# Performance work log

Measured on AMD Instinct MI355X. Metric: run time of the kernel, lower is better.

The kernel has to match this reference:

```python
import jax, jax.numpy as jnp
import numpy as np

N, E, IN, HID, G, OUT = 50000, 800000, 9, 128, 256, 10
CLUSTERS, NCO, MCO = 20, 6, 4  # numerator deg 5 (6 coeffs), denominator deg 4
EPS = 1e-5


def _gcn(x, W, b, src, dst):
    # PyG GCNConv: x' = D^-1/2 (A + I) D^-1/2 (x W) + b, with self-loops
    n = x.shape[0]
    h = x @ W  # [N, out]
    ones = jnp.ones(src.shape[0], h.dtype)
    deg = jax.ops.segment_sum(ones, dst, num_segments=n) + 1.0  # + self-loop
    dinv = jax.lax.rsqrt(deg)
    coef = (dinv[src] * dinv[dst])[:, None]
    agg = jax.ops.segment_sum(h[src] * coef, dst, num_segments=n)
    agg = agg + h * (dinv * dinv)[:, None]  # self-loop messages
    return agg + b


def _rational(x, num, den, assign):
    # per-cluster safe Pade rational: P_5(x) / (1 + |Q_4(x)|), coeffs gathered per channel
    a = num[assign]  # [HID, 6]
    q = den[assign]  # [HID, 4]
    P = a[:, 5]
    for i in (4, 3, 2, 1, 0):
        P = P * x + a[:, i]
    Q = q[:, 3]
    for i in (2, 1, 0):
        Q = Q * x + q[:, i]
    Q = Q * x  # Q has no constant term
    return P / (1.0 + jnp.abs(Q))


def _bn(x, g, b):
    m = x.mean(axis=0)
    v = x.var(axis=0)
    return g * (x - m) * jax.lax.rsqrt(v + EPS) + b


def setup_inputs() -> dict:
    key = jax.random.key(0)
    ks = jax.random.split(key, 32)
    d = {}
    d["x"] = jax.random.normal(ks[0], (N, IN), jnp.float32)
    d["edge_index"] = jax.random.randint(ks[1], (2, E), 0, N, jnp.int32)
    d["batch"] = jnp.sort(jax.random.randint(ks[2], (N,), 0, G, jnp.int32))
    dims = [(IN, HID), (HID, HID), (HID, HID), (HID, HID)]
    for i, (di, do) in enumerate(dims):
        d[f"W{i}"] = jax.random.normal(ks[3 + i], (di, do), jnp.float32) / np.sqrt(di)
        d[f"b{i}"] = jnp.zeros((do,), jnp.float32)
        d[f"g{i}"] = jnp.ones((do,), jnp.float32)
        d[f"be{i}"] = jnp.zeros((do,), jnp.float32)
    d["rat_num"] = jax.random.normal(ks[10], (CLUSTERS, NCO), jnp.float32) * 0.3
    d["rat_den"] = jax.random.normal(ks[11], (CLUSTERS, MCO), jnp.float32) * 0.3
    d["cluster_assign"] = (jnp.arange(HID) % CLUSTERS).astype(jnp.int32)
    d["HW1"] = jax.random.normal(ks[12], (HID, HID), jnp.float32) / np.sqrt(HID)
    d["Hb1"] = jnp.zeros((HID,), jnp.float32)
    d["HW2"] = jax.random.normal(ks[13], (HID, HID), jnp.float32) / np.sqrt(HID)
    d["Hb2"] = jnp.zeros((HID,), jnp.float32)
    d["HW3"] = jax.random.normal(ks[14], (HID, OUT), jnp.float32) / np.sqrt(HID)
    d["Hb3"] = jnp.zeros((OUT,), jnp.float32)
    return d


def reference(x, edge_index, batch,
              W0, b0, g0, be0, W1, b1, g1, be1,
              W2, b2, g2, be2, W3, b3, g3, be3,
              rat_num, rat_den, cluster_assign,
              HW1, Hb1, HW2, Hb2, HW3, Hb3):
    src, dst = edge_index[0], edge_index[1]
    h = x
    for W, b, g, be in ((W0, b0, g0, be0), (W1, b1, g1, be1),
                        (W2, b2, g2, be2), (W3, b3, g3, be3)):
        h = _gcn(h, W, b, src, dst)
        h = _rational(h, rat_num, rat_den, cluster_assign)
        h = _bn(h, g, be)
        # Dropout(p=0.1): identity in eval mode
    # global mean pool over graphs
    counts = jax.ops.segment_sum(jnp.ones((h.shape[0],), h.dtype), batch, num_segments=G)
    pooled = jax.ops.segment_sum(h, batch, num_segments=G) / jnp.maximum(counts, 1.0)[:, None]
    # MLP head: (Dropout->Linear->GELU) x2, Dropout->Linear
    z = jax.nn.gelu(pooled @ HW1 + Hb1, approximate=False)
    z = jax.nn.gelu(z @ HW2 + Hb2, approximate=False)
    return z @ HW3 + Hb3
```

## Files before the change

kernel.cpp:

```cpp
#include <hip/hip_runtime.h>
#include <math.h>

#define HID 128
#define GRP 256
#define INF 9
#define OUTF 10
#define NPART 8

typedef _Float16 half8 __attribute__((ext_vector_type(8)));
typedef _Float16 h2 __attribute__((ext_vector_type(2)));
typedef __attribute__((ext_vector_type(4))) float f32x4;

__device__ __forceinline__ int2 nt_load_int2(const int2* p) {
    long long v = __builtin_nontemporal_load((const long long*)p);
    int2 r; r.x = (int)(v & 0xffffffffLL); r.y = (int)(v >> 32);
    return r;
}

__global__ void hist_prepw_kernel(const int* __restrict__ ei, int* __restrict__ cnt_part,
                                  int E, int n,
                                  const float* __restrict__ W1, const float* __restrict__ W2,
                                  const float* __restrict__ W3,
                                  _Float16* __restrict__ Whi, _Float16* __restrict__ Wlo) {
    int e = blockIdx.x * 256 + threadIdx.x;
    if (e < E) atomicAdd(&cnt_part[(size_t)(blockIdx.x & 7) * n + ei[E + e]], 1);
    if (blockIdx.x < 192) {
        int l = blockIdx.x >> 6;
        int idx = (blockIdx.x & 63) * 256 + threadIdx.x;
        const float* W = (l == 0) ? W1 : (l == 1) ? W2 : W3;
        int nn = idx >> 7, k = idx & 127;
        float w = W[k * HID + nn];
        _Float16 hi = (_Float16)w;
        _Float16 lo = (_Float16)(w - (float)hi);
        int nt = nn >> 4, l16 = nn & 15;
        int kc = k >> 5, quad = (k >> 3) & 3, j = k & 7;
        size_t off = (size_t)(l + 1) * HID * HID +
                     ((((nt * 4 + kc) * 4 + quad) * 16 + l16) * 8 + j);
        Whi[off] = hi;
        Wlo[off] = lo;
    }
}

__global__ __launch_bounds__(256) void scanA_kernel(const int* __restrict__ cnt_part,
                                                    int* __restrict__ bsum, int n) {
    int tid = threadIdx.x;
    int base = blockIdx.x * 1024 + tid * 4;
    int s = 0;
    #pragma unroll
    for (int i = 0; i < 4; i++) {
        int idx = base + i;
        if (idx < n) {
            #pragma unroll
            for (int x = 0; x < NPART; x++) s += cnt_part[(size_t)x * n + idx];
        }
    }
    #pragma unroll
    for (int off = 32; off > 0; off >>= 1) s += __shfl_down(s, off);
    __shared__ int ws[4];
    if ((tid & 63) == 0) ws[tid >> 6] = s;
    __syncthreads();
    if (tid == 0) bsum[blockIdx.x] = ws[0] + ws[1] + ws[2] + ws[3];
}

__global__ void scanB_kernel(int* __restrict__ bsum, int* __restrict__ row_ptr,
                             int nb, int n) {
    int lane = threadIdx.x;
    int carry = 0;
    for (int base = 0; base < nb; base += 64) {
        int v = (base + lane < nb) ? bsum[base + lane] : 0;
        int ps = v;
        #pragma unroll
        for (int off = 1; off < 64; off <<= 1) {
            int t = __shfl_up(ps, off);
            if (lane >= off) ps += t;
        }
        if (base + lane < nb) bsum[base + lane] = carry + ps - v;
        carry += __shfl(ps, 63);
    }
    if (lane == 0) row_ptr[n] = carry;
}

__global__ __launch_bounds__(256) void scanC_kernel(const int* __restrict__ cnt_part,
                                                    const int* __restrict__ bsum,
                                                    const int* __restrict__ batch,
                                                    int* __restrict__ row_ptr,
                                                    int* __restrict__ cursor_part,
                                                    float* __restrict__ dinv,
                                                    int* __restrict__ gstart,
                                                    int* __restrict__ gend, int n) {
    int tid = threadIdx.x;
    int lane = tid & 63, wid = tid >> 6;
    int idx0 = blockIdx.x * 1024 + tid * 4;
    int v[4];
    #pragma unroll
    for (int i = 0; i < 4; i++) {
        int idx = idx0 + i;
        int s = 0;
        if (idx < n) {
            #pragma unroll
            for (int x = 0; x < NPART; x++) s += cnt_part[(size_t)x * n + idx];
        }
        v[i] = s;
    }
    int s = v[0] + v[1] + v[2] + v[3];
    int ps = s;
    #pragma unroll
    for (int off = 1; off < 64; off <<= 1) {
        int t = __shfl_up(ps, off);
        if (lane >= off) ps += t;
    }
    __shared__ int wsum[4];
    if (lane == 63) wsum[wid] = ps;
    __syncthreads();
    int woff = 0;
    #pragma unroll
    for (int i = 0; i < 4; i++) if (i < wid) woff += wsum[i];
    int run = bsum[blockIdx.x] + woff + (ps - s);
    #pragma unroll
    for (int i = 0; i < 4; i++) {
        int idx = idx0 + i;
        if (idx < n) {
            row_ptr[idx] = run;
            dinv[idx] = rsqrtf((float)(v[i] + 1));
            int b = run;
            #pragma unroll
            for (int x = 0; x < NPART; x++) {
                cursor_part[(size_t)x * n + idx] = b;
                b += cnt_part[(size_t)x * n + idx];
            }
            run += v[i];
            int bt = batch[idx];
            if (idx == 0 || batch[idx - 1] != bt) gstart[bt] = idx;
            if (idx == n - 1 || batch[idx + 1] != bt) gend[bt] = idx + 1;
        }
    }
}

__global__ void fill_kernel(const int* __restrict__ ei, int* __restrict__ cursor_part,
                            const float* __restrict__ dinv,
                            int2* __restrict__ csr, int E, int n) {
    int e = blockIdx.x * blockDim.x + threadIdx.x;
    if (e >= E) return;
    int s = ei[e], d = ei[E + e];
    int pos = atomicAdd(&cursor_part[(size_t)(blockIdx.x & 7) * n + d], 1);
    long long v = ((long long)__float_as_int(dinv[s] * dinv[d]) << 32) | (unsigned)s;
    *(long long*)&csr[pos] = v;
}

__global__ __launch_bounds__(256) void statreduce_kernel(const float* __restrict__ part,
                                                         int nb, float* __restrict__ statOut) {
    int j = blockIdx.x;
    int tid = threadIdx.x;
    float s = 0.0f;
    for (int b = tid; b < nb; b += 256) s += part[(size_t)b * 256 + j];
    #pragma unroll
    for (int off = 32; off > 0; off >>= 1) s += __shfl_down(s, off);
    __shared__ float ws[4];
    if ((tid & 63) == 0) ws[tid >> 6] = s;
    __syncthreads();
    if (tid == 0) statOut[j] = ws[0] + ws[1] + ws[2] + ws[3];
}

__device__ __forceinline__ float rational_act(float xv, const float* __restrict__ a,
                                              const float* __restrict__ q) {
    float P = a[5];
    P = fmaf(P, xv, a[4]); P = fmaf(P, xv, a[3]); P = fmaf(P, xv, a[2]);
    P = fmaf(P, xv, a[1]); P = fmaf(P, xv, a[0]);
    float Q = q[3];
    Q = fmaf(Q, xv, q[2]); Q = fmaf(Q, xv, q[1]); Q = fmaf(Q, xv, q[0]);
    Q *= xv;
    return P / (1.0f + fabsf(Q));
}

__global__ __launch_bounds__(256) void aggx_kernel(const float* __restrict__ x,
                                                   const int* __restrict__ row_ptr,
                                                   const int2* __restrict__ csr,
                                                   const float* __restrict__ dinv,
                                                   float* __restrict__ aggX,
                                                   float* __restrict__ cagg, int n) {
    int tid = threadIdx.x;
    int node = blockIdx.x * 16 + (tid >> 4);
    int lane = tid & 15;
    if (node >= n) return;
    float di = dinv[node];
    float self = di * di;
    float acc = (lane < INF) ? x[node * INF + lane] * self : 0.0f;
    float cfs = self;
    int beg = row_ptr[node], end = row_ptr[node + 1];
    for (int j = beg; j < end; j++) {
        int2 p = nt_load_int2(&csr[j]);
        float cf = __int_as_float(p.y);
        cfs += cf;
        if (lane < INF) acc = fmaf(cf, x[p.x * INF + lane], acc);
    }
    if (lane < INF) aggX[node * INF + lane] = acc;
    if (lane == 0) cagg[node] = cfs;
}

__global__ __launch_bounds__(256) void gemm0_fused_kernel(const float* __restrict__ aggX,
                                                          const float* __restrict__ W0,
                                                          const float* __restrict__ b0,
                                                          const float* __restrict__ rat_num,
                                                          const float* __restrict__ rat_den,
                                                          const int* __restrict__ cl_assign,
                                                          _Float16* __restrict__ act,
                                                          float* __restrict__ part, int n) {
    __shared__ float Ws[INF * HID];
    __shared__ float s_num[120], s_den[80];
    __shared__ int s_cl[HID];
    __shared__ float s_b[HID];
    __shared__ float s_sum[HID], s_sq[HID];
    int tid = threadIdx.x;
    for (int i = tid; i < INF * HID; i += 256) Ws[i] = W0[i];
    if (tid < 120) s_num[tid] = rat_num[tid];
    if (tid < 80) s_den[tid] = rat_den[tid];
    if (tid < HID) {
        s_cl[tid] = cl_assign[tid];
        s_b[tid] = b0[tid];
        s_sum[tid] = 0.0f; s_sq[tid] = 0.0f;
    }
    __syncthreads();
    int w = tid >> 6, lane = tid & 63;
    int c0 = lane * 2, c1 = c0 + 1;
    const float* a0 = s_num + s_cl[c0] * 6;
    const float* q0 = s_den + s_cl[c0] * 4;
    const float* a1 = s_num + s_cl[c1] * 6;
    const float* q1 = s_den + s_cl[c1] * 4;
    float psum0 = 0.0f, psq0 = 0.0f, psum1 = 0.0f, psq1 = 0.0f;
    for (int node = blockIdx.x * 4 + w; node < n; node += gridDim.x * 4) {
        float xv[INF];
        #pragma unroll
        for (int k = 0; k < INF; k++) xv[k] = aggX[node * INF + k];
        float acc0 = s_b[c0], acc1 = s_b[c1];
        #pragma unroll
        for (int k = 0; k < INF; k++) {
            acc0 = fmaf(xv[k], Ws[k * HID + c0], acc0);
            acc1 = fmaf(xv[k], Ws[k * HID + c1], acc1);
        }
        float r0 = rational_act(acc0, a0, q0);
        float r1 = rational_act(acc1, a1, q1);
        h2 o; o[0] = (_Float16)r0; o[1] = (_Float16)r1;
        __builtin_nontemporal_store(o, (h2*)&act[(size_t)node * HID + c0]);
        psum0 += r0; psq0 = fmaf(r0, r0, psq0);
        psum1 += r1; psq1 = fmaf(r1, r1, psq1);
    }
    atomicAdd(&s_sum[c0], psum0);
    atomicAdd(&s_sq[c0], psq0);
    atomicAdd(&s_sum[c1], psum1);
    atomicAdd(&s_sq[c1], psq1);
    __syncthreads();
    float pv = (tid < 128) ? s_sum[tid] : s_sq[tid - 128];
    __builtin_nontemporal_store(pv, &part[(size_t)blockIdx.x * 256 + tid]);
}

__global__ __launch_bounds__(256, 5) void layer_fused_kernel(const _Float16* __restrict__ act,
                                                          const int2* __restrict__ csr,
                                                          const int* __restrict__ row_ptr,
                                                          const float* __restrict__ dinv,
                                                          const float* __restrict__ cagg,
                                                          const float* __restrict__ statPrev,
                                                          const float* __restrict__ gPrev,
                                                          const float* __restrict__ bePrev,
                                                          const _Float16* __restrict__ Whi,
                                                          const _Float16* __restrict__ Wlo,
                                                          const float* __restrict__ bias,
                                                          const float* __restrict__ rat_num,
                                                          const float* __restrict__ rat_den,
                                                          const int* __restrict__ cl_assign,
                                                          _Float16* __restrict__ actOut,
                                                          float* __restrict__ part, int n) {
    __shared__ _Float16 Alds[16 * 136];
    __shared__ float s_bnw[HID], s_bnu[HID];
    __shared__ float s_num[120], s_den[80];
    __shared__ int s_cl[HID];
    __shared__ float s_bias[HID];
    __shared__ float s_sum[HID], s_sq[HID];
    int tid = threadIdx.x;
    if (tid < 120) s_num[tid] = rat_num[tid];
    if (tid < 80) s_den[tid] = rat_den[tid];
    if (tid < HID) {
        float inv_n = 1.0f / (float)n;
        float mean = statPrev[tid] * inv_n;
        float var = statPrev[HID + tid] * inv_n - mean * mean;
        float w = gPrev[tid] * rsqrtf(var + 1e-5f);
        s_bnw[tid] = w;
        s_bnu[tid] = bePrev[tid] - mean * w;
        s_cl[tid] = cl_assign[tid];
        s_bias[tid] = bias[tid];
        s_sum[tid] = 0.0f; s_sq[tid] = 0.0f;
    }
    __syncthreads();

    int r0 = blockIdx.x * 16;
    int grp = tid >> 4, glane = tid & 15;
    int grpbase = tid & 48;
    const half8* act8 = (const half8*)act;

    int node = r0 + grp;
    int beg = 0, end = 0;
    if (node < n) { beg = row_ptr[node]; end = row_ptr[node + 1]; }
    int2 pfirst = make_int2(0, 0); float cfirst = 0.0f;
    {
        int rem = end - beg;
        if (rem > 0) {
            int m = rem < 16 ? rem : 16;
            int2 p = nt_load_int2(&csr[beg + (glane < m ? glane : m - 1)]);
            pfirst = p;
            cfirst = (glane < m) ? __int_as_float(p.y) : 0.0f;
        }
    }

    #define PROCESS8(off)                                                              \
        {                                                                              \
            int srcs[8]; float cfs[8];                                                 \
            _Pragma("unroll")                                                          \
            for (int u = 0; u < 8; u++) {                                              \
                srcs[u] = __shfl(cp.x, grpbase + (off) + u, 64);                       \
                cfs[u]  = __shfl(cc,   grpbase + (off) + u, 64);                       \
            }                                                                          \
            half8 v[8];                                                                \
            _Pragma("unroll")                                                          \
            for (int u = 0; u < 8; u++) v[u] = act8[srcs[u] * 16 + glane];             \
            _Pragma("unroll")                                                          \
            for (int u = 0; u < 8; u++) {                                              \
                _Pragma("unroll")                                                      \
                for (int t = 0; t < 8; t++)                                            \
                    acc[t] = fmaf(cfs[u], (float)v[u][t], acc[t]);                     \
            }                                                                          \
        }

    {
        half8 o;
        if (node < n) {
            float di = dinv[node];
            float selfc = di * di;
            half8 sv = act8[node * 16 + glane];
            float acc[8];
            #pragma unroll
            for (int t = 0; t < 8; t++) acc[t] = (float)sv[t] * selfc;
            int base = beg;
            if (base < end) {
                int2 cp = pfirst; float cc = cfirst;
                for (;;) {
                    int m = end - base; if (m > 16) m = 16;
                    PROCESS8(0)
                    if (m > 8) PROCESS8(8)
                    base += 16;
                    if (base >= end) break;
                    int mn = end - base; if (mn > 16) mn = 16;
                    int2 p = nt_load_int2(&csr[base + (glane < mn ? glane : mn - 1)]);
                    cp = p;
                    cc = (glane < mn) ? __int_as_float(p.y) : 0.0f;
                }
            }
            float cg = cagg[node];
            #pragma unroll
            for (int t = 0; t < 8; t++) {
                int c = glane * 8 + t;
                o[t] = (_Float16)fmaf(s_bnw[c], acc[t], s_bnu[c] * cg);
            }
        } else {
            #pragma unroll
            for (int t = 0; t < 8; t++) o[t] = (_Float16)0.0f;
        }
        *(half8*)&Alds[grp * 136 + glane * 8] = o;
    }
    #undef PROCESS8
    __syncthreads();

    int w = tid >> 6, l64 = tid & 63;
    int quad = l64 >> 4, l16 = l64 & 15;
    const half8* Bh8 = (const half8*)Whi;
    const half8* Bl8 = (const half8*)Wlo;
    f32x4 acc[2];
    #pragma unroll
    for (int j = 0; j < 2; j++) acc[j] = (f32x4){0.f, 0.f, 0.f, 0.f};
    #pragma unroll
    for (int kc = 0; kc < 4; kc++) {
        half8 a = *(const half8*)&Alds[l16 * 136 + kc * 32 + quad * 8];
        #pragma unroll
        for (int j = 0; j < 2; j++) {
            int ntg = w * 2 + j;
            half8 bh = Bh8[(ntg * 4 + kc) * 64 + l64];
            half8 bl = Bl8[(ntg * 4 + kc) * 64 + l64];
            acc[j] = __builtin_amdgcn_mfma_f32_16x16x32_f16(a, bh, acc[j], 0, 0, 0);
            acc[j] = __builtin_amdgcn_mfma_f32_16x16x32_f16(a, bl, acc[j], 0, 0, 0);
        }
    }
    __syncthreads();

    float ps[2], pq[2];
    #pragma unroll
    for (int j = 0; j < 2; j++) { ps[j] = 0.0f; pq[j] = 0.0f; }
    #pragma unroll
    for (int reg = 0; reg < 4; reg++) {
        int lrow = quad * 4 + reg;
        int row = r0 + lrow;
        bool live = (row < n);
        #pragma unroll
        for (int j = 0; j < 2; j++) {
            int col = (w * 2 + j) * 16 + l16;
            float v = acc[j][reg] + s_bias[col];
            float r = rational_act(v, s_num + s_cl[col] * 6, s_den + s_cl[col] * 4);
            Alds[lrow * 136 + col] = (_Float16)r;
            if (live) { ps[j] += r; pq[j] = fmaf(r, r, pq[j]); }
        }
    }
    #pragma unroll
    for (int j = 0; j < 2; j++) {
        float a2 = ps[j] + __shfl_xor(ps[j], 16, 64);
        a2 += __shfl_xor(a2, 32, 64);
        float b2 = pq[j] + __shfl_xor(pq[j], 16, 64);
        b2 += __shfl_xor(b2, 32, 64);
        if (quad == 0) {
            int col = (w * 2 + j) * 16 + l16;
            atomicAdd(&s_sum[col], a2);
            atomicAdd(&s_sq[col], b2);
        }
    }
    __syncthreads();
    {
        float pv = (tid < 128) ? s_sum[tid] : s_sq[tid - 128];
        __builtin_nontemporal_store(pv, &part[(size_t)blockIdx.x * 256 + tid]);
    }
    {
        int lrow = tid >> 4, lc = (tid & 15) * 8;
        int row = r0 + lrow;
        if (row < n) {
            half8 v = *(const half8*)&Alds[lrow * 136 + lc];
            __builtin_nontemporal_store(v, (half8*)&actOut[(size_t)row * HID + lc]);
        }
    }
}

__global__ __launch_bounds__(256) void poolmlp_kernel(const _Float16* __restrict__ act,
                                                      const int* __restrict__ gstart,
                                                      const int* __restrict__ gend,
                                                      const float* __restrict__ stat,
                                                      const float* __restrict__ g3,
                                                      const float* __restrict__ be3,
                                                      const float* __restrict__ HW1,
                                                      const float* __restrict__ Hb1,
                                                      const float* __restrict__ HW2,
                                                      const float* __restrict__ Hb2,
                                                      const float* __restrict__ HW3,
                                                      const float* __restrict__ Hb3,
                                                      float* __restrict__ out, int n) {
    __shared__ float red[16][HID];
    __shared__ float s_pool[HID];
    __shared__ float s_z[HID];
    int gi = blockIdx.x;
    int tid = threadIdx.x;
    int rg = tid >> 4, lane = tid & 15;
    int s = gstart[gi], e = gend[gi];
    const half8* act8 = (const half8*)act;
    float a[8];
    #pragma unroll
    for (int t = 0; t < 8; t++) a[t] = 0.0f;
    for (int r = s + rg; r < e; r += 16) {
        half8 v = act8[r * 16 + lane];
        #pragma unroll
        for (int t = 0; t < 8; t++) a[t] += (float)v[t];
    }
    #pragma unroll
    for (int t = 0; t < 8; t++) red[rg][lane * 8 + t] = a[t];
    __syncthreads();
    if (tid < HID) {
        float tot = 0.0f;
        #pragma unroll
        for (int i = 0; i < 16; i++) tot += red[i][tid];
        int cnt = e - s;
        float pooled = 0.0f;
        if (cnt > 0) {
            float inv_n = 1.0f / (float)n;
            float mean = stat[tid] * inv_n;
            float var = stat[HID + tid] * inv_n - mean * mean;
            float w = g3[tid] * rsqrtf(var + 1e-5f);
            float u = be3[tid] - mean * w;
            pooled = fmaf(w, tot / (float)cnt, u);
        }
        s_pool[tid] = pooled;
    }
    __syncthreads();
    if (tid < HID) {
        float acc = Hb1[tid];
        #pragma unroll 8
        for (int k = 0; k < HID; k++) acc = fmaf(s_pool[k], HW1[k * HID + tid], acc);
        s_z[tid] = 0.5f * acc * (1.0f + erff(acc * 0.70710678118654752f));
    }
    __syncthreads();
    if (tid < HID) {
        float acc = Hb2[tid];
        #pragma unroll 8
        for (int k = 0; k < HID; k++) acc = fmaf(s_z[k], HW2[k * HID + tid], acc);
        s_pool[tid] = 0.5f * acc * (1.0f + erff(acc * 0.70710678118654752f));
    }
    __syncthreads();
    if (tid < OUTF) {
        float acc = Hb3[tid];
        #pragma unroll 8
        for (int k = 0; k < HID; k++) acc = fmaf(s_pool[k], HW3[k * OUTF + tid], acc);
        out[gi * OUTF + tid] = acc;
    }
}

extern "C" void kernel_launch(void* const* d_in, const int* in_sizes, int n_in,
                              void* d_out, int out_size, void* d_ws, size_t ws_size,
                              hipStream_t stream) {
    const float* x          = (const float*)d_in[0];
    const int*   edge_index = (const int*)d_in[1];
    const int*   batch      = (const int*)d_in[2];
    const float* W[4]  = {(const float*)d_in[3], (const float*)d_in[7], (const float*)d_in[11], (const float*)d_in[15]};
    const float* bL[4] = {(const float*)d_in[4], (const float*)d_in[8], (const float*)d_in[12], (const float*)d_in[16]};
    const float* gL[4] = {(const float*)d_in[5], (const float*)d_in[9], (const float*)d_in[13], (const float*)d_in[17]};
    const float* beL[4]= {(const float*)d_in[6], (const float*)d_in[10], (const float*)d_in[14], (const float*)d_in[18]};
    const float* rat_num = (const float*)d_in[19];
    const float* rat_den = (const float*)d_in[20];
    const int*   cl_assign = (const int*)d_in[21];
    const float* HW1 = (const float*)d_in[22];
    const float* Hb1 = (const float*)d_in[23];
    const float* HW2 = (const float*)d_in[24];
    const float* Hb2 = (const float*)d_in[25];
    const float* HW3 = (const float*)d_in[26];
    const float* Hb3 = (const float*)d_in[27];
    float* out = (float*)d_out;

    const int N = in_sizes[0] / INF;
    const int E = in_sizes[1] / 2;
    const int NB = (N + 1023) / 1024;
    const int layer_grid = (N + 15) / 16;

    char* wsb = (char*)d_ws;
    size_t o = 0;
    #define ALIGNB o = (o + 63) & ~(size_t)63;
    int*   cnt_part = (int*)(wsb + o * 4);  o += (size_t)NPART * N; ALIGNB
    int*   gstart  = (int*)(wsb + o * 4);  o += GRP; ALIGNB
    int*   gend    = (int*)(wsb + o * 4);  o += GRP; ALIGNB
    float* bnstat  = (float*)(wsb + o * 4); o += 4 * 256; ALIGNB
    size_t zero_elems = o;
    int*   bsum    = (int*)(wsb + o * 4);  o += ((NB + 63) & ~63); ALIGNB
    int*   cursor_part = (int*)(wsb + o * 4);  o += (size_t)NPART * N; ALIGNB
    int*   row_ptr = (int*)(wsb + o * 4);  o += N + 1; ALIGNB
    float* dinv    = (float*)(wsb + o * 4); o += N; ALIGNB
    float* cagg    = (float*)(wsb + o * 4); o += N; ALIGNB
    int2*  csr     = (int2*)(wsb + o * 4);  o += 2 * (size_t)E; ALIGNB
    float* aggX    = (float*)(wsb + o * 4); o += (size_t)N * INF; ALIGNB
    _Float16* WhiAll = (_Float16*)(wsb + o * 4); o += 4 * HID * HID / 2; ALIGNB
    _Float16* WloAll = (_Float16*)(wsb + o * 4); o += 4 * HID * HID / 2; ALIGNB
    _Float16* actA  = (_Float16*)(wsb + o * 4); o += (size_t)N * HID / 2; ALIGNB
    _Float16* actB  = (_Float16*)(wsb + o * 4); o += (size_t)N * HID / 2; ALIGNB
    float* part    = (float*)(wsb + o * 4); o += (size_t)layer_grid * 256;

    hipMemsetAsync(d_ws, 0, zero_elems * 4, stream);

    int eb = (E + 255) / 256;
    hist_prepw_kernel<<<eb, 256, 0, stream>>>(edge_index, cnt_part, E, N, W[1], W[2], W[3],
                                              WhiAll, WloAll);
    scanA_kernel<<<NB, 256, 0, stream>>>(cnt_part, bsum, N);
    scanB_kernel<<<1, 64, 0, stream>>>(bsum, row_ptr, NB, N);
    scanC_kernel<<<NB, 256, 0, stream>>>(cnt_part, bsum, batch, row_ptr, cursor_part, dinv,
                                         gstart, gend, N);
    fill_kernel<<<eb, 256, 0, stream>>>(edge_index, cursor_part, dinv, csr, E, N);

    aggx_kernel<<<(N + 15) / 16, 256, 0, stream>>>(x, row_ptr, csr, dinv, aggX, cagg, N);
    gemm0_fused_kernel<<<1024, 256, 0, stream>>>(aggX, W[0], bL[0], rat_num, rat_den,
                                                 cl_assign, actA, part, N);
    statreduce_kernel<<<256, 256, 0, stream>>>(part, 1024, bnstat);

    _Float16* ain = actA;
    _Float16* aout = actB;
    for (int l = 1; l < 4; l++) {
        layer_fused_kernel<<<layer_grid, 256, 0, stream>>>(ain, csr, row_ptr, dinv, cagg,
                                                           bnstat + (l - 1) * 256,
                                                           gL[l - 1], beL[l - 1],
                                                           WhiAll + (size_t)l * HID * HID,
                                                           WloAll + (size_t)l * HID * HID,
                                                           bL[l], rat_num, rat_den, cl_assign,
                                                           aout, part, N);
        statreduce_kernel<<<256, 256, 0, stream>>>(part, layer_grid, bnstat + l * 256);
        _Float16* t = ain; ain = aout; aout = t;
    }
    poolmlp_kernel<<<GRP, 256, 0, stream>>>(ain, gstart, gend, bnstat + 3 * 256,
                                            gL[3], beL[3], HW1, Hb1, HW2, Hb2, HW3, Hb3,
                                            out, N);
}
```

Measured before the change: 426.3 us.

## Fuse layer-0 aggregation into gemm0 and fold block-sum scan into scanC

Removes the single-block scanB kernel: each scanC block now sums the preceding block totals itself, and the last node writes row_ptr[n]. Also fuses the aggx aggregation into gemm0, so each 16-thread group aggregates one node's 9 input features, shares them by shuffle, and computes 8 output channels. This drops the aggX round trip through memory and two launches. In exchange, shared-memory atomics for the batch-norm stats rise to one per channel per node, and the partial-stat grid grows from 1024 to layer_grid blocks, so statreduce has more partials to sum.

Measured after the change: 485.9 us. 1.14x slower.

```diff
diff --git a/kernel.cpp b/kernel.cpp
--- a/kernel.cpp
+++ b/kernel.cpp
@@ -62,24 +62,6 @@
     if (tid == 0) bsum[blockIdx.x] = ws[0] + ws[1] + ws[2] + ws[3];
 }
 
-__global__ void scanB_kernel(int* __restrict__ bsum, int* __restrict__ row_ptr,
-                             int nb, int n) {
-    int lane = threadIdx.x;
-    int carry = 0;
-    for (int base = 0; base < nb; base += 64) {
-        int v = (base + lane < nb) ? bsum[base + lane] : 0;
-        int ps = v;
-        #pragma unroll
-        for (int off = 1; off < 64; off <<= 1) {
-            int t = __shfl_up(ps, off);
-            if (lane >= off) ps += t;
-        }
-        if (base + lane < nb) bsum[base + lane] = carry + ps - v;
-        carry += __shfl(ps, 63);
-    }
-    if (lane == 0) row_ptr[n] = carry;
-}
-
 __global__ __launch_bounds__(256) void scanC_kernel(const int* __restrict__ cnt_part,
                                                     const int* __restrict__ bsum,
                                                     const int* __restrict__ batch,
@@ -109,13 +91,19 @@
         int t = __shfl_up(ps, off);
         if (lane >= off) ps += t;
     }
+    int pv = (tid < blockIdx.x) ? bsum[tid] : 0;
+    #pragma unroll
+    for (int off = 32; off > 0; off >>= 1) pv += __shfl_down(pv, off);
     __shared__ int wsum[4];
+    __shared__ int wpre[4];
     if (lane == 63) wsum[wid] = ps;
-    __syncthreads();
+    if (lane == 0) wpre[wid] = pv;
+    __syncthreads();
+    int pre = wpre[0] + wpre[1] + wpre[2] + wpre[3];
     int woff = 0;
     #pragma unroll
     for (int i = 0; i < 4; i++) if (i < wid) woff += wsum[i];
-    int run = bsum[blockIdx.x] + woff + (ps - s);
+    int run = pre + woff + (ps - s);
     #pragma unroll
     for (int i = 0; i < 4; i++) {
         int idx = idx0 + i;
@@ -131,7 +119,10 @@
             run += v[i];
             int bt = batch[idx];
             if (idx == 0 || batch[idx - 1] != bt) gstart[bt] = idx;
-            if (idx == n - 1 || batch[idx + 1] != bt) gend[bt] = idx + 1;
+            if (idx == n - 1 || batch[idx + 1] != bt) {
+                gend[bt] = idx + 1;
+            }
+            if (idx == n - 1) row_ptr[n] = run;
         }
     }
 }
@@ -172,38 +163,17 @@
     return P / (1.0f + fabsf(Q));
 }
 
-__global__ __launch_bounds__(256) void aggx_kernel(const float* __restrict__ x,
-                                                   const int* __restrict__ row_ptr,
-                                                   const int2* __restrict__ csr,
-                                                   const float* __restrict__ dinv,
-                                                   float* __restrict__ aggX,
-                                                   float* __restrict__ cagg, int n) {
-    int tid = threadIdx.x;
-    int node = blockIdx.x * 16 + (tid >> 4);
-    int lane = tid & 15;
-    if (node >= n) return;
-    float di = dinv[node];
-    float self = di * di;
-    float acc = (lane < INF) ? x[node * INF + lane] * self : 0.0f;
-    float cfs = self;
-    int beg = row_ptr[node], end = row_ptr[node + 1];
-    for (int j = beg; j < end; j++) {
-        int2 p = nt_load_int2(&csr[j]);
-        float cf = __int_as_float(p.y);
-        cfs += cf;
-        if (lane < INF) acc = fmaf(cf, x[p.x * INF + lane], acc);
-    }
-    if (lane < INF) aggX[node * INF + lane] = acc;
-    if (lane == 0) cagg[node] = cfs;
-}
-
-__global__ __launch_bounds__(256) void gemm0_fused_kernel(const float* __restrict__ aggX,
+__global__ __launch_bounds__(256) void gemm0_fused_kernel(const float* __restrict__ x,
+                                                          const int* __restrict__ row_ptr,
+                                                          const int2* __restrict__ csr,
+                                                          const float* __restrict__ dinv,
                                                           const float* __restrict__ W0,
                                                           const float* __restrict__ b0,
                                                           const float* __restrict__ rat_num,
                                                           const float* __restrict__ rat_den,
                                                           const int* __restrict__ cl_assign,
                                                           _Float16* __restrict__ act,
+                                                          float* __restrict__ cagg,
                                                           float* __restrict__ part, int n) {
     __shared__ float Ws[INF * HID];
     __shared__ float s_num[120], s_den[80];
@@ -220,34 +190,42 @@
         s_sum[tid] = 0.0f; s_sq[tid] = 0.0f;
     }
     __syncthreads();
-    int w = tid >> 6, lane = tid & 63;
-    int c0 = lane * 2, c1 = c0 + 1;
-    const float* a0 = s_num + s_cl[c0] * 6;
-    const float* q0 = s_den + s_cl[c0] * 4;
-    const float* a1 = s_num + s_cl[c1] * 6;
-    const float* q1 = s_den + s_cl[c1] * 4;
-    float psum0 = 0.0f, psq0 = 0.0f, psum1 = 0.0f, psq1 = 0.0f;
-    for (int node = blockIdx.x * 4 + w; node < n; node += gridDim.x * 4) {
-        float xv[INF];
+    int grp = tid >> 4, glane = tid & 15;
+    int grpbase = tid & 48;
+    int node = blockIdx.x * 16 + grp;
+    float accv = 0.0f, cfs = 0.0f;
+    if (node < n) {
+        float di = dinv[node];
+        float self = di * di;
+        accv = (glane < INF) ? x[node * INF + glane] * self : 0.0f;
+        cfs = self;
+        int beg = row_ptr[node], end = row_ptr[node + 1];
+        for (int j = beg; j < end; j++) {
+            int2 p = nt_load_int2(&csr[j]);
+            float cf = __int_as_float(p.y);
+            cfs += cf;
+            if (glane < INF) accv = fmaf(cf, x[p.x * INF + glane], accv);
+        }
+        if (glane == 0) cagg[node] = cfs;
+    }
+    float av[INF];
+    #pragma unroll
+    for (int k = 0; k < INF; k++) av[k] = __shfl(accv, grpbase + k, 64);
+    if (node < n) {
+        half8 o;
         #pragma unroll
-        for (int k = 0; k < INF; k++) xv[k] = aggX[node * INF + k];
-        float acc0 = s_b[c0], acc1 = s_b[c1];
-        #pragma unroll
-        for (int k = 0; k < INF; k++) {
-            acc0 = fmaf(xv[k], Ws[k * HID + c0], acc0);
-            acc1 = fmaf(xv[k], Ws[k * HID + c1], acc1);
-        }
-        float r0 = rational_act(acc0, a0, q0);
-        float r1 = rational_act(acc1, a1, q1);
-        h2 o; o[0] = (_Float16)r0; o[1] = (_Float16)r1;
-        __builtin_nontemporal_store(o, (h2*)&act[(size_t)node * HID + c0]);
-        psum0 += r0; psq0 = fmaf(r0, r0, psq0);
-        psum1 += r1; psq1 = fmaf(r1, r1, psq1);
-    }
-    atomicAdd(&s_sum[c0], psum0);
-    atomicAdd(&s_sq[c0], psq0);
-    atomicAdd(&s_sum[c1], psum1);
-    atomicAdd(&s_sq[c1], psq1);
+        for (int t = 0; t < 8; t++) {
+            int c = glane * 8 + t;
+            float acc = s_b[c];
+            #pragma unroll
+            for (int k = 0; k < INF; k++) acc = fmaf(av[k], Ws[k * HID + c], acc);
+            float r = rational_act(acc, s_num + s_cl[c] * 6, s_den + s_cl[c] * 4);
+            o[t] = (_Float16)r;
+            atomicAdd(&s_sum[c], r);
+            atomicAdd(&s_sq[c], r * r);
+        }
+        __builtin_nontemporal_store(o, (half8*)&act[(size_t)node * HID + glane * 8]);
+    }
     __syncthreads();
     float pv = (tid < 128) ? s_sum[tid] : s_sq[tid - 128];
     __builtin_nontemporal_store(pv, &part[(size_t)blockIdx.x * 256 + tid]);
@@ -544,7 +522,6 @@
     float* dinv    = (float*)(wsb + o * 4); o += N; ALIGNB
     float* cagg    = (float*)(wsb + o * 4); o += N; ALIGNB
     int2*  csr     = (int2*)(wsb + o * 4);  o += 2 * (size_t)E; ALIGNB
-    float* aggX    = (float*)(wsb + o * 4); o += (size_t)N * INF; ALIGNB
     _Float16* WhiAll = (_Float16*)(wsb + o * 4); o += 4 * HID * HID / 2; ALIGNB
     _Float16* WloAll = (_Float16*)(wsb + o * 4); o += 4 * HID * HID / 2; ALIGNB
     _Float16* actA  = (_Float16*)(wsb + o * 4); o += (size_t)N * HID / 2; ALIGNB
@@ -557,15 +534,14 @@
     hist_prepw_kernel<<<eb, 256, 0, stream>>>(edge_index, cnt_part, E, N, W[1], W[2], W[3],
                                               WhiAll, WloAll);
     scanA_kernel<<<NB, 256, 0, stream>>>(cnt_part, bsum, N);
-    scanB_kernel<<<1, 64, 0, stream>>>(bsum, row_ptr, NB, N);
     scanC_kernel<<<NB, 256, 0, stream>>>(cnt_part, bsum, batch, row_ptr, cursor_part, dinv,
                                          gstart, gend, N);
     fill_kernel<<<eb, 256, 0, stream>>>(edge_index, cursor_part, dinv, csr, E, N);
 
-    aggx_kernel<<<(N + 15) / 16, 256, 0, stream>>>(x, row_ptr, csr, dinv, aggX, cagg, N);
-    gemm0_fused_kernel<<<1024, 256, 0, stream>>>(aggX, W[0], bL[0], rat_num, rat_den,
-                                                 cl_assign, actA, part, N);
-    statreduce_kernel<<<256, 256, 0, stream>>>(part, 1024, bnstat);
+    gemm0_fused_kernel<<<layer_grid, 256, 0, stream>>>(x, row_ptr, csr, dinv, W[0], bL[0],
+                                                       rat_num, rat_den, cl_assign,
+                                                       actA, cagg, part, N);
+    statreduce_kernel<<<256, 256, 0, stream>>>(part, layer_grid, bnstat);
 
     _Float16* ain = actA;
     _Float16* aout = actB;
@@ -576,7 +552,7 @@
                                                            WhiAll + (size_t)l * HID * HID,
                                                            WloAll + (size_t)l * HID * HID,
                                                            bL[l], rat_num, rat_den, cl_assign,
-                                                           aout, part, N);
+                                                           aout, bnstat ? part : part, N);
         statreduce_kernel<<<256, 256, 0, stream>>>(part, layer_grid, bnstat + l * 256);
         _Float16* t = ain; ain = aout; aout = t;
     }
```
